# Performance work log

Hardware: AMD Instinct MI355X
Metric: run time of the kernel (lower is better)

Reference implementation:

```python
import jax, jax.numpy as jnp
import numpy as np

B, S = 2048, 256
V, E, H, LAT, NL = 4, 8, 64, 3, 2
NT = V + 2          # vocab + start + pad tokens
START = V
TEMP = 1.0


def setup_inputs() -> dict:
    key = jax.random.key(0)
    ks = jax.random.split(key, 32)
    def p(k, shape, scale=0.1):
        return jax.random.normal(k, shape, jnp.float32) * scale
    return {
        "tokens": jax.random.randint(ks[0], (B, S), 0, V),
        "emb": p(ks[1], (NT, E)),
        "enc_Wih0": p(ks[2], (3 * H, E)), "enc_Whh0": p(ks[3], (3 * H, H)),
        "enc_bih0": p(ks[4], (3 * H,)), "enc_bhh0": p(ks[5], (3 * H,)),
        "enc_Wih1": p(ks[6], (3 * H, H)), "enc_Whh1": p(ks[7], (3 * H, H)),
        "enc_bih1": p(ks[8], (3 * H,)), "enc_bhh1": p(ks[9], (3 * H,)),
        "fc_mu_W": p(ks[10], (LAT, H)), "fc_mu_b": p(ks[11], (LAT,)),
        "fc_var_W": p(ks[12], (LAT, H)), "fc_var_b": p(ks[13], (LAT,)),
        "dec_emb": p(ks[14], (NT, H)),
        "proj_W": p(ks[15], (H, LAT)), "proj_b": p(ks[16], (H,)),
        "dec_Wih0": p(ks[17], (3 * H, H)), "dec_Whh0": p(ks[18], (3 * H, H)),
        "dec_bih0": p(ks[19], (3 * H,)), "dec_bhh0": p(ks[20], (3 * H,)),
        "dec_Wih1": p(ks[21], (3 * H, H)), "dec_Whh1": p(ks[22], (3 * H, H)),
        "dec_bih1": p(ks[23], (3 * H,)), "dec_bhh1": p(ks[24], (3 * H,)),
        "head_W": p(ks[25], (V, H)), "head_b": p(ks[26], (V,)),
    }


def gru_cell(h, x, Wih, Whh, bih, bhh):
    # PyTorch GRU gate order: reset, update, new
    gi = x @ Wih.T + bih            # [B, 3H]
    gh = h @ Whh.T + bhh            # [B, 3H]
    ir, iz, ig = jnp.split(gi, 3, axis=-1)
    hr, hz, hg = jnp.split(gh, 3, axis=-1)
    r = jax.nn.sigmoid(ir + hr)
    z = jax.nn.sigmoid(iz + hz)
    n = jnp.tanh(ig + r * hg)
    return (1.0 - z) * n + z * h


def run_gru_layer(x, Wih, Whh, bih, bhh):
    # x: [B, S, D] -> (outputs [B, S, H], final hidden [B, H])
    def step(h, xt):
        h2 = gru_cell(h, xt, Wih, Whh, bih, bhh)
        return h2, h2
    h0 = jnp.zeros((x.shape[0], Whh.shape[1]), x.dtype)
    hT, ys = jax.lax.scan(step, h0, x.transpose(1, 0, 2))
    return ys.transpose(1, 0, 2), hT


def reference(tokens, emb, enc_Wih0, enc_Whh0, enc_bih0, enc_bhh0,
              enc_Wih1, enc_Whh1, enc_bih1, enc_bhh1,
              fc_mu_W, fc_mu_b, fc_var_W, fc_var_b,
              dec_emb, proj_W, proj_b,
              dec_Wih0, dec_Whh0, dec_bih0, dec_bhh0,
              dec_Wih1, dec_Whh1, dec_bih1, dec_bhh1,
              head_W, head_b):
    b, s = tokens.shape
    # ---- encode ----
    x = emb[tokens]                                   # [B, S, E]
    seq, _ = run_gru_layer(x, enc_Wih0, enc_Whh0, enc_bih0, enc_bhh0)
    _, h_last = run_gru_layer(seq, enc_Wih1, enc_Whh1, enc_bih1, enc_bhh1)
    mu = h_last @ fc_mu_W.T + fc_mu_b                 # [B, LAT]
    log_var = h_last @ fc_var_W.T + fc_var_b          # [B, LAT]
    # ---- reparameterize ----
    eps = jax.random.normal(jax.random.key(1), mu.shape, mu.dtype)
    z = eps * jnp.exp(0.5 * log_var) + mu
    hz = z @ proj_W.T + proj_b                        # [B, H]; same init for both layers
    tok0 = jnp.full((b,), START, jnp.int32)
    keys = jax.random.split(jax.random.key(2), s)
    def step(carry, k):
        h0, h1, tok = carry
        xe = dec_emb[tok]                             # [B, H]
        h0n = gru_cell(h0, xe, dec_Wih0, dec_Whh0, dec_bih0, dec_bhh0)
        h1n = gru_cell(h1, h0n, dec_Wih1, dec_Whh1, dec_bih1, dec_bhh1)
        logits = (h1n @ head_W.T + head_b) / TEMP     # [B, V]
        probs = jax.nn.softmax(logits, axis=-1)
        nt = jax.random.categorical(k, logits)        # multinomial sample (detached)
        return (h0n, h1n, nt), probs
    _, probs_seq = jax.lax.scan(step, (hz, hz, tok0), keys)   # [S, B, V]
    recons = probs_seq.transpose(1, 0, 2)[:, :, None, :]      # [B, S, 1, V]
    return recons, tokens, mu, log_var
```

## Files before the change

### kernel.cpp

```cpp
#include <hip/hip_runtime.h>
#include <stdint.h>

typedef unsigned int u32;
typedef unsigned short u16;

#define NB   2048
#define SS   256
#define HH   64
#define VV   4
#define LATD 3
#define NTHR 512

#define TOK_OFF (NB*SS*VV)
#define MU_OFF  (TOK_OFF + NB*SS)
#define LV_OFF  (MU_OFF + NB*LATD)

__device__ __forceinline__ void tf2x32(u32 k0, u32 k1, u32 x0, u32 x1, u32& o0, u32& o1){
  u32 k2 = k0 ^ k1 ^ 0x1BD11BDAu;
  x0 += k0; x1 += k1;
#define TFR(r) { x0 += x1; x1 = (x1<<r)|(x1>>(32-r)); x1 ^= x0; }
  TFR(13) TFR(15) TFR(26) TFR(6)   x0 += k1; x1 += k2 + 1u;
  TFR(17) TFR(29) TFR(16) TFR(24)  x0 += k2; x1 += k0 + 2u;
  TFR(13) TFR(15) TFR(26) TFR(6)   x0 += k0; x1 += k1 + 3u;
  TFR(17) TFR(29) TFR(16) TFR(24)  x0 += k1; x1 += k2 + 4u;
  TFR(13) TFR(15) TFR(26) TFR(6)   x0 += k2; x1 += k0 + 5u;
#undef TFR
  o0 = x0; o1 = x1;
}
__device__ __forceinline__ u32 foldb(u32 k0, u32 k1, u32 i){
  u32 a,b; tf2x32(k0,k1,0u,i,a,b); return a^b;
}
__device__ __forceinline__ float b2u(u32 bits){
  union{u32 i;float f;}c; c.i = (bits>>9) | 0x3f800000u; return c.f - 1.0f;
}
__device__ __forceinline__ float erfinv_f(float x){
  float w = -log1pf(-x*x);
  float p;
  if (w < 5.0f){
    w -= 2.5f;
    p = 2.81022636e-08f;
    p = fmaf(p,w, 3.43273939e-07f);
    p = fmaf(p,w,-3.5233877e-06f);
    p = fmaf(p,w,-4.39150654e-06f);
    p = fmaf(p,w, 0.00021858087f);
    p = fmaf(p,w,-0.00125372503f);
    p = fmaf(p,w,-0.00417768164f);
    p = fmaf(p,w, 0.246640727f);
    p = fmaf(p,w, 1.50140941f);
  } else {
    w = sqrtf(w) - 3.0f;
    p = -0.000200214257f;
    p = fmaf(p,w, 0.000100950558f);
    p = fmaf(p,w, 0.00134934322f);
    p = fmaf(p,w,-0.00367342844f);
    p = fmaf(p,w, 0.00573950773f);
    p = fmaf(p,w,-0.0076224613f);
    p = fmaf(p,w, 0.00943887047f);
    p = fmaf(p,w, 1.00167406f);
    p = fmaf(p,w, 2.83297682f);
  }
  return p*x;
}
__device__ __forceinline__ float sigm(float x){ return 1.0f/(1.0f+expf(-x)); }
__device__ __forceinline__ float rl(float x, int l){
  return __int_as_float(__builtin_amdgcn_readlane(__float_as_int(x), l));
}
__device__ __forceinline__ float wred(float x){
  #pragma unroll
  for (int m=1; m<64; m<<=1) x += __shfl_xor(x, m, 64);
  return x;
}

#define MATVEC1R(Wr, Wz, Wn, xv, ar, az, an)                                   \
  _Pragma("unroll")                                                            \
  for (int k4 = 0; k4 < 16; k4++){                                             \
    float4 wr = Wr[k4];                                                        \
    float4 wz = Wz[k4];                                                        \
    float4 wn = Wn[k4];                                                        \
    float x0 = rl(xv, 4*k4), x1 = rl(xv, 4*k4+1), x2 = rl(xv, 4*k4+2), x3 = rl(xv, 4*k4+3); \
    ar = fmaf(wr.x,x0,ar); ar = fmaf(wr.y,x1,ar); ar = fmaf(wr.z,x2,ar); ar = fmaf(wr.w,x3,ar); \
    az = fmaf(wz.x,x0,az); az = fmaf(wz.y,x1,az); az = fmaf(wz.z,x2,az); az = fmaf(wz.w,x3,az); \
    an = fmaf(wn.x,x0,an); an = fmaf(wn.y,x1,an); an = fmaf(wn.z,x2,an); an = fmaf(wn.w,x3,an); \
  }

#define MATVEC1L(W, xv, ar, az, an)                                            \
  _Pragma("unroll 2")                                                          \
  for (int k4 = 0; k4 < 16; k4++){                                             \
    float4 wr = W[k4*192 + j];                                                 \
    float4 wz = W[k4*192 + 64 + j];                                            \
    float4 wn = W[k4*192 + 128 + j];                                           \
    float x0 = rl(xv, 4*k4), x1 = rl(xv, 4*k4+1), x2 = rl(xv, 4*k4+2), x3 = rl(xv, 4*k4+3); \
    ar = fmaf(wr.x,x0,ar); ar = fmaf(wr.y,x1,ar); ar = fmaf(wr.z,x2,ar); ar = fmaf(wr.w,x3,ar); \
    az = fmaf(wz.x,x0,az); az = fmaf(wz.y,x1,az); az = fmaf(wz.z,x2,az); az = fmaf(wz.w,x3,az); \
    an = fmaf(wn.x,x0,an); an = fmaf(wn.y,x1,an); an = fmaf(wn.z,x2,an); an = fmaf(wn.w,x3,an); \
  }

#define LOAD_REG_W(G, Ar, Az, An)                                              \
  _Pragma("unroll")                                                            \
  for (int k4 = 0; k4 < 16; k4++){                                             \
    Ar[k4] = G[(j)*16 + k4];                                                   \
    Az[k4] = G[(64 + j)*16 + k4];                                              \
    An[k4] = G[(128 + j)*16 + k4];                                             \
  }

#define PIN4(v) asm volatile("" : "+v"(v.x), "+v"(v.y), "+v"(v.z), "+v"(v.w))
#define PIN_W(Ar, Az, An)                                                      \
  _Pragma("unroll")                                                            \
  for (int k4 = 0; k4 < 16; k4++){ PIN4(Ar[k4]); PIN4(Az[k4]); PIN4(An[k4]); }

__global__ __launch_bounds__(NTHR, 2) void enc_kernel(
    const int* __restrict__ tokens, const float* __restrict__ emb,
    const float* __restrict__ Wih0, const float* __restrict__ Whh0,
    const float* __restrict__ bih0, const float* __restrict__ bhh0,
    const float* __restrict__ Wih1, const float* __restrict__ Whh1,
    const float* __restrict__ bih1, const float* __restrict__ bhh1,
    const float* __restrict__ muW, const float* __restrict__ mub,
    const float* __restrict__ vaW, const float* __restrict__ vab,
    const float* __restrict__ pW,  const float* __restrict__ pb,
    float* __restrict__ out, float* __restrict__ hz_ws)
{
  __shared__ float4 wi1[16*192];
  __shared__ float4 wh1[16*192];
  __shared__ float tokT[VV*192];

  const int tid = threadIdx.x;
  const int b0  = blockIdx.x * 8;
  const int j   = tid & 63;
  const int wv  = tid >> 6;
  const int row = b0 + wv;

  for (int i4 = tid; i4 < 3072; i4 += NTHR){
    int g = i4 >> 4, k4 = i4 & 15;
    wi1[k4*192 + g] = ((const float4*)Wih1)[i4];
    wh1[k4*192 + g] = ((const float4*)Whh1)[i4];
  }
  if (tid < 192){
    #pragma unroll
    for (int v = 0; v < VV; v++){
      float acc = 0.0f;
      #pragma unroll
      for (int e = 0; e < 8; e++) acc = fmaf(emb[v*8+e], Wih0[tid*8+e], acc);
      tokT[v*192 + tid] = acc + bih0[tid];
    }
  }
  for (int i = tid; i < 8*SS; i += NTHR){
    int rr = i >> 8, tq = i & 255;
    out[TOK_OFF + (b0+rr)*SS + tq] = (float)tokens[(b0+rr)*SS + tq];
  }

  float4 w0r[16], w0z[16], w0n[16];
  {
    const float4* G0 = (const float4*)Whh0;
    LOAD_REG_W(G0, w0r, w0z, w0n)
    PIN_W(w0r, w0z, w0n)
  }
  __syncthreads();

  const float bhr0 = bhh0[j], bhz0 = bhh0[64+j], bhn0 = bhh0[128+j];
  const float bir1 = bih1[j], biz1 = bih1[64+j], bin1 = bih1[128+j];
  const float bhr1 = bhh1[j], bhz1 = bhh1[64+j], bhn1 = bhh1[128+j];

  float h0 = 0.0f, h1 = 0.0f;
  const int tR = row*SS;

  for (int t = 0; t < SS; t++){
    asm volatile("" ::: "memory");
    int k = tokens[tR + t];
    float ar=0, az=0, an=0;
    MATVEC1R(w0r, w0z, w0n, h0, ar, az, an)
    {
      float ir = tokT[k*192+j], iz = tokT[k*192+64+j], ig = tokT[k*192+128+j];
      float rg = sigm(ir + ar + bhr0);
      float zg = sigm(iz + az + bhz0);
      float ng = tanhf(ig + rg*(an + bhn0));
      h0 = (1.0f - zg)*ng + zg*h0;
    }
    float air=0, aiz=0, ain=0, ahr=0, ahz=0, ahn=0;
    MATVEC1L(wi1, h0, air, aiz, ain)
    MATVEC1L(wh1, h1, ahr, ahz, ahn)
    {
      float rg = sigm(air + bir1 + ahr + bhr1);
      float zg = sigm(aiz + biz1 + ahz + bhz1);
      float ng = tanhf(ain + bin1 + rg*(ahn + bhn1));
      h1 = (1.0f - zg)*ng + zg*h1;
    }
  }

  const float LO_ = -0.99999994f;
  {
    float hv = h1;
    int gb = row;
    float mu0,mu1,mu2, lv0,lv1,lv2;
    { float pm = muW[0*64+j]*hv; pm = wred(pm); mu0 = pm + mub[0];
      float pv = vaW[0*64+j]*hv; pv = wred(pv); lv0 = pv + vab[0]; }
    { float pm = muW[1*64+j]*hv; pm = wred(pm); mu1 = pm + mub[1];
      float pv = vaW[1*64+j]*hv; pv = wred(pv); lv1 = pv + vab[1]; }
    { float pm = muW[2*64+j]*hv; pm = wred(pm); mu2 = pm + mub[2];
      float pv = vaW[2*64+j]*hv; pv = wred(pv); lv2 = pv + vab[2]; }
    if (j < 3){
      float mv  = (j==0)?mu0:(j==1)?mu1:mu2;
      float lvv = (j==0)?lv0:(j==1)?lv1:lv2;
      out[MU_OFF + gb*LATD + j] = mv;
      out[LV_OFF + gb*LATD + j] = lvv;
    }
    float z0,z1,z2;
    #pragma unroll
    for (int l = 0; l < 3; l++){
      u32 bits = foldb(0u, 1u, (u32)(gb*LATD + l));
      float u01 = b2u(bits);
      float uu = u01 * 2.0f;
      uu = uu + LO_;
      uu = fmaxf(LO_, uu);
      float ep = 1.41421354f * erfinv_f(uu);
      float lvv = (l==0)?lv0:(l==1)?lv1:lv2;
      float mvv = (l==0)?mu0:(l==1)?mu1:mu2;
      float zv = ep * expf(0.5f*lvv) + mvv;
      if (l==0) z0 = zv; else if (l==1) z1 = zv; else z2 = zv;
    }
    float hzj = pW[j*3+0]*z0;
    hzj += pW[j*3+1]*z1;
    hzj += pW[j*3+2]*z2;
    hzj += pb[j];
    hz_ws[gb*HH + j] = hzj;
  }
}

__global__ __launch_bounds__(NTHR, 2) void dec_kernel(
    const float* __restrict__ demb,
    const float* __restrict__ Wih0, const float* __restrict__ Whh0,
    const float* __restrict__ bih0, const float* __restrict__ bhh0,
    const float* __restrict__ Wih1, const float* __restrict__ Whh1,
    const float* __restrict__ bih1, const float* __restrict__ bhh1,
    const float* __restrict__ headW, const float* __restrict__ headb,
    const float* __restrict__ hz_ws, float* __restrict__ out)
{
  __shared__ float4 wi1[16*192];
  __shared__ float4 wh1[16*192];
  __shared__ float decT[6*192];
  __shared__ u32 sk0[SS], sk1[SS];

  const int tid = threadIdx.x;
  const int b0  = blockIdx.x * 8;
  const int j   = tid & 63;
  const int wv  = tid >> 6;
  const int row = b0 + wv;

  for (int i4 = tid; i4 < 3072; i4 += NTHR){
    int g = i4 >> 4, k4 = i4 & 15;
    wi1[k4*192 + g] = ((const float4*)Wih1)[i4];
    wh1[k4*192 + g] = ((const float4*)Whh1)[i4];
  }
  if (tid < 192){
    #pragma unroll
    for (int v = 0; v < 6; v++){
      float acc = 0.0f;
      #pragma unroll 8
      for (int k = 0; k < 64; k++) acc = fmaf(demb[v*64+k], Wih0[tid*64+k], acc);
      decT[v*192 + tid] = acc + bih0[tid];
    }
  }
  if (tid < SS){
    u32 a,b; tf2x32(0u, 2u, 0u, (u32)tid, a, b);
    sk0[tid] = a; sk1[tid] = b;
  }

  float4 w0r[16], w0z[16], w0n[16];
  {
    const float4* G0 = (const float4*)Whh0;
    LOAD_REG_W(G0, w0r, w0z, w0n)
    PIN_W(w0r, w0z, w0n)
  }
  __syncthreads();

  const float bhr0 = bhh0[j], bhz0 = bhh0[64+j], bhn0 = bhh0[128+j];
  const float bir1 = bih1[j], biz1 = bih1[64+j], bin1 = bih1[128+j];
  const float bhr1 = bhh1[j], bhz1 = bhh1[64+j], bhn1 = bhh1[128+j];
  const float hw0 = headW[0*64+j], hw1 = headW[1*64+j], hw2 = headW[2*64+j], hw3 = headW[3*64+j];
  const float hb0 = headb[0], hb1 = headb[1], hb2 = headb[2], hb3 = headb[3];

  float h0 = hz_ws[row*HH + j];
  float h1 = h0;
  int tk = 4;

  const int vv = j & 3;
  const float TINY = 1.17549435e-38f;

  for (int t = 0; t < SS; t++){
    asm volatile("" ::: "memory");
    float ar=0, az=0, an=0;
    MATVEC1R(w0r, w0z, w0n, h0, ar, az, an)
    {
      float ir = decT[tk*192+j], iz = decT[tk*192+64+j], ig = decT[tk*192+128+j];
      float rg = sigm(ir + ar + bhr0);
      float zg = sigm(iz + az + bhz0);
      float ng = tanhf(ig + rg*(an + bhn0));
      h0 = (1.0f - zg)*ng + zg*h0;
    }
    float air=0, aiz=0, ain=0, ahr=0, ahz=0, ahn=0;
    MATVEC1L(wi1, h0, air, aiz, ain)
    MATVEC1L(wh1, h1, ahr, ahz, ahn)
    {
      float rg = sigm(air + bir1 + ahr + bhr1);
      float zg = sigm(aiz + biz1 + ahz + bhz1);
      float ng = tanhf(ain + bin1 + rg*(ahn + bhn1));
      h1 = (1.0f - zg)*ng + zg*h1;
    }
    float l0 = wred(hw0*h1) + hb0;
    float l1 = wred(hw1*h1) + hb1;
    float l2 = wred(hw2*h1) + hb2;
    float l3 = wred(hw3*h1) + hb3;
    float lg = (vv==0)?l0:(vv==1)?l1:(vv==2)?l2:l3;
    u32 bits = foldb(sk0[t], sk1[t], (u32)(row*VV + vv));
    float u01 = b2u(bits);
    float u = u01 + TINY;
    u = fmaxf(TINY, u);
    float gmb = -logf(-logf(u));
    float prt = lg + gmb;
    float mx = lg;
    mx = fmaxf(mx, __shfl_xor(mx, 1, 64));
    mx = fmaxf(mx, __shfl_xor(mx, 2, 64));
    float e = expf(lg - mx);
    float se = e;
    se += __shfl_xor(se, 1, 64);
    se += __shfl_xor(se, 2, 64);
    float prob = e / se;
    float bp = prt; int bv = vv;
    { float o = __shfl_xor(bp, 1, 64); int ov = __shfl_xor(bv, 1, 64);
      if (o > bp || (o == bp && ov < bv)){ bp = o; bv = ov; } }
    { float o = __shfl_xor(bp, 2, 64); int ov = __shfl_xor(bv, 2, 64);
      if (o > bp || (o == bp && ov < bv)){ bp = o; bv = ov; } }
    if (j < 4) out[(size_t)row*SS*VV + (size_t)t*VV + vv] = prob;
    tk = __builtin_amdgcn_readlane(bv, 0);
  }
}

extern "C" void kernel_launch(void* const* d_in, const int* in_sizes, int n_in,
                              void* d_out, int out_size, void* d_ws, size_t ws_size,
                              hipStream_t stream){
  const int*   tokens = (const int*)d_in[0];
  const float* emb    = (const float*)d_in[1];
  const float* eWih0  = (const float*)d_in[2];  const float* eWhh0 = (const float*)d_in[3];
  const float* ebih0  = (const float*)d_in[4];  const float* ebhh0 = (const float*)d_in[5];
  const float* eWih1  = (const float*)d_in[6];  const float* eWhh1 = (const float*)d_in[7];
  const float* ebih1  = (const float*)d_in[8];  const float* ebhh1 = (const float*)d_in[9];
  const float* muW    = (const float*)d_in[10]; const float* mub   = (const float*)d_in[11];
  const float* vaW    = (const float*)d_in[12]; const float* vab   = (const float*)d_in[13];
  const float* demb   = (const float*)d_in[14];
  const float* pW     = (const float*)d_in[15]; const float* pb    = (const float*)d_in[16];
  const float* dWih0  = (const float*)d_in[17]; const float* dWhh0 = (const float*)d_in[18];
  const float* dbih0  = (const float*)d_in[19]; const float* dbhh0 = (const float*)d_in[20];
  const float* dWih1  = (const float*)d_in[21]; const float* dWhh1 = (const float*)d_in[22];
  const float* dbih1  = (const float*)d_in[23]; const float* dbhh1 = (const float*)d_in[24];
  const float* hWp    = (const float*)d_in[25]; const float* hbp   = (const float*)d_in[26];
  float* out = (float*)d_out;
  float* hz = (float*)d_ws;

  enc_kernel<<<NB/8, NTHR, 0, stream>>>(tokens, emb,
      eWih0, eWhh0, ebih0, ebhh0, eWih1, eWhh1, ebih1, ebhh1,
      muW, mub, vaW, vab, pW, pb, out, hz);
  dec_kernel<<<NB/8, NTHR, 0, stream>>>(demb,
      dWih0, dWhh0, dbih0, dbhh0, dWih1, dWhh1, dbih1, dbhh1,
      hWp, hbp, hz, out);
}
```

Measured before the change: 2.648 ms.

## Precompute Gumbel noise in LDS, register-cache token table, merge head reductions

Gumbel noise for all timesteps and the block's eight rows is now generated in the prologue and stored in shared memory, which removes the threefry fold and two logs from the serial per-step path. The decoder input-gate table is cached in registers and selected by token with a select chain instead of an LDS load. The four head-logit wave reductions are merged into one butterfly that reduces partially and then selects per lane. The PIN_W register pinning is dropped, which may change how the weights are allocated to registers. The 32KB Gumbel buffer raises LDS use, which could limit occupancy.

```diff
diff --git a/kernel.cpp b/kernel.cpp
--- a/kernel.cpp
+++ b/kernel.cpp
@@ -237,13 +237,14 @@
   __shared__ float4 wi1[16*192];
   __shared__ float4 wh1[16*192];
   __shared__ float decT[6*192];
-  __shared__ u32 sk0[SS], sk1[SS];
+  __shared__ float gum[SS*32];
 
   const int tid = threadIdx.x;
   const int b0  = blockIdx.x * 8;
   const int j   = tid & 63;
   const int wv  = tid >> 6;
   const int row = b0 + wv;
+  const float TINY = 1.17549435e-38f;
 
   for (int i4 = tid; i4 < 3072; i4 += NTHR){
     int g = i4 >> 4, k4 = i4 & 15;
@@ -259,38 +260,51 @@
       decT[v*192 + tid] = acc + bih0[tid];
     }
   }
-  if (tid < SS){
-    u32 a,b; tf2x32(0u, 2u, 0u, (u32)tid, a, b);
-    sk0[tid] = a; sk1[tid] = b;
+  for (int idx = tid; idx < SS*32; idx += NTHR){
+    int t  = idx >> 5;
+    int rv = idx & 31;
+    u32 a,b; tf2x32(0u, 2u, 0u, (u32)t, a, b);
+    u32 bits = foldb(a, b, (u32)((b0 + (rv>>2))*VV + (rv&3)));
+    float u01 = b2u(bits);
+    float u = fmaxf(TINY, u01 + TINY);
+    gum[idx] = -logf(-logf(u));
   }
 
   float4 w0r[16], w0z[16], w0n[16];
   {
     const float4* G0 = (const float4*)Whh0;
     LOAD_REG_W(G0, w0r, w0z, w0n)
-    PIN_W(w0r, w0z, w0n)
   }
   __syncthreads();
+
+  float dTr[6], dTz[6], dTn[6];
+  #pragma unroll
+  for (int v = 0; v < 6; v++){
+    dTr[v] = decT[v*192 + j];
+    dTz[v] = decT[v*192 + 64 + j];
+    dTn[v] = decT[v*192 + 128 + j];
+  }
 
   const float bhr0 = bhh0[j], bhz0 = bhh0[64+j], bhn0 = bhh0[128+j];
   const float bir1 = bih1[j], biz1 = bih1[64+j], bin1 = bih1[128+j];
   const float bhr1 = bhh1[j], bhz1 = bhh1[64+j], bhn1 = bhh1[128+j];
   const float hw0 = headW[0*64+j], hw1 = headW[1*64+j], hw2 = headW[2*64+j], hw3 = headW[3*64+j];
-  const float hb0 = headb[0], hb1 = headb[1], hb2 = headb[2], hb3 = headb[3];
+  const int vv = j & 3;
+  const float hbv = (vv==0)?headb[0]:(vv==1)?headb[1]:(vv==2)?headb[2]:headb[3];
 
   float h0 = hz_ws[row*HH + j];
   float h1 = h0;
   int tk = 4;
 
-  const int vv = j & 3;
-  const float TINY = 1.17549435e-38f;
-
   for (int t = 0; t < SS; t++){
     asm volatile("" ::: "memory");
+    float gmb = gum[t*32 + (wv<<2) + vv];
     float ar=0, az=0, an=0;
     MATVEC1R(w0r, w0z, w0n, h0, ar, az, an)
     {
-      float ir = decT[tk*192+j], iz = decT[tk*192+64+j], ig = decT[tk*192+128+j];
+      float ir = (tk==0)?dTr[0]:(tk==1)?dTr[1]:(tk==2)?dTr[2]:(tk==3)?dTr[3]:(tk==4)?dTr[4]:dTr[5];
+      float iz = (tk==0)?dTz[0]:(tk==1)?dTz[1]:(tk==2)?dTz[2]:(tk==3)?dTz[3]:(tk==4)?dTz[4]:dTz[5];
+      float ig = (tk==0)?dTn[0]:(tk==1)?dTn[1]:(tk==2)?dTn[2]:(tk==3)?dTn[3]:(tk==4)?dTn[4]:dTn[5];
       float rg = sigm(ir + ar + bhr0);
       float zg = sigm(iz + az + bhz0);
       float ng = tanhf(ig + rg*(an + bhn0));
@@ -305,16 +319,17 @@
       float ng = tanhf(ain + bin1 + rg*(ahn + bhn1));
       h1 = (1.0f - zg)*ng + zg*h1;
     }
-    float l0 = wred(hw0*h1) + hb0;
-    float l1 = wred(hw1*h1) + hb1;
-    float l2 = wred(hw2*h1) + hb2;
-    float l3 = wred(hw3*h1) + hb3;
-    float lg = (vv==0)?l0:(vv==1)?l1:(vv==2)?l2:l3;
-    u32 bits = foldb(sk0[t], sk1[t], (u32)(row*VV + vv));
-    float u01 = b2u(bits);
-    float u = u01 + TINY;
-    u = fmaxf(TINY, u);
-    float gmb = -logf(-logf(u));
+    float a0 = hw0*h1, a1 = hw1*h1, a2 = hw2*h1, a3 = hw3*h1;
+    a0 += __shfl_xor(a0, 1, 64); a0 += __shfl_xor(a0, 2, 64);
+    a1 += __shfl_xor(a1, 1, 64); a1 += __shfl_xor(a1, 2, 64);
+    a2 += __shfl_xor(a2, 1, 64); a2 += __shfl_xor(a2, 2, 64);
+    a3 += __shfl_xor(a3, 1, 64); a3 += __shfl_xor(a3, 2, 64);
+    float s = (vv==0)?a0:(vv==1)?a1:(vv==2)?a2:a3;
+    s += __shfl_xor(s, 4, 64);
+    s += __shfl_xor(s, 8, 64);
+    s += __shfl_xor(s, 16, 64);
+    s += __shfl_xor(s, 32, 64);
+    float lg = s + hbv;
     float prt = lg + gmb;
     float mx = lg;
     mx = fmaxf(mx, __shfl_xor(mx, 1, 64));
```

Result: no change. 2.681 ms (+1.2%).
